# Performance work log

Hardware: AMD Instinct MI355X
Metric: run time of the kernel (lower is better)

The kernel has to match this reference:

```python
import jax, jax.numpy as jnp
import numpy as np

WIN = 16
SIGMA = 1.5
DATA_RANGE = 255.0
C1 = (0.01 * DATA_RANGE) ** 2
C2 = (0.03 * DATA_RANGE) ** 2
MSE_W = 0.7
SSIM_W = 0.3


def _gauss_window(channels):
    # 16x16 gaussian window, sigma=1.5, normalized to sum 1
    coords = np.arange(WIN, dtype=np.float32) - (WIN - 1) / 2.0
    g = np.exp(-(coords ** 2) / (2.0 * SIGMA ** 2))
    g = g / g.sum()
    w2d = np.outer(g, g)  # [16,16]
    w = np.broadcast_to(w2d, (channels, 1, WIN, WIN)).copy()
    return jnp.asarray(w)


def _depthwise_conv(x, w):
    # x: [B,C,H,W], w: [C,1,k,k] depthwise, VALID padding
    return jax.lax.conv_general_dilated(
        x, w, window_strides=(1, 1), padding='VALID',
        dimension_numbers=('NCHW', 'OIHW', 'NCHW'),
        feature_group_count=x.shape[1])


def _ssim(img1, img2):
    # images assumed in [0,255] (PIL-equivalent range)
    C = img1.shape[1]
    w = _gauss_window(C).astype(img1.dtype)
    mu1 = _depthwise_conv(img1, w)
    mu2 = _depthwise_conv(img2, w)
    mu1_sq = mu1 * mu1
    mu2_sq = mu2 * mu2
    mu12 = mu1 * mu2
    sigma1_sq = _depthwise_conv(img1 * img1, w) - mu1_sq
    sigma2_sq = _depthwise_conv(img2 * img2, w) - mu2_sq
    sigma12 = _depthwise_conv(img1 * img2, w) - mu12
    ssim_map = ((2.0 * mu12 + C1) * (2.0 * sigma12 + C2)) / (
        (mu1_sq + mu2_sq + C1) * (sigma1_sq + sigma2_sq + C2))
    # per-sample mean, then mean over batch (matches batch_ssim loop + .mean())
    return jnp.mean(ssim_map, axis=(1, 2, 3)).mean()


def setup_inputs() -> dict:
    key = jax.random.key(0)
    k1, k2 = jax.random.split(key)
    shape = (32, 3, 512, 512)
    output = jax.random.uniform(k1, shape, dtype=jnp.float32)
    target = jax.random.uniform(k2, shape, dtype=jnp.float32)
    return {'output': output, 'target': target}


def reference(output, target):
    mse_loss = jnp.mean((output - target) ** 2)
    # to_pil_image scales [0,1] float tensors to [0,255] uint8; SSIM computed
    # in 0-255 range with data_range=255
    ssim_val = _ssim(output * 255.0, target * 255.0)
    ssim_loss = 1.0 - ssim_val
    return mse_loss * MSE_W + ssim_loss * SSIM_W
```

## Files before the change

kernel.cpp:

```cpp
#include <hip/hip_runtime.h>
#include <math.h>
#include <string.h>

typedef __attribute__((ext_vector_type(8))) short bf16x8;
typedef __attribute__((ext_vector_type(4))) float f32x4;

namespace {
constexpr int TOUT = 32;
constexpr int IMG  = 512;
constexpr int HALO = 15;
constexpr int OUTW = IMG - HALO;
constexpr int NBLK = 16 * 16 * 96;

struct WinPk { unsigned w[8]; };

__device__ __forceinline__ unsigned prm(unsigned hi, unsigned lo) {
    return __builtin_amdgcn_perm(hi, lo, 0x07060302u);
}
}

template <bool TWO_STAGE>
__global__ __launch_bounds__(256)
void ssim_mse_kernel(const float* __restrict__ img1,
                     const float* __restrict__ img2,
                     WinPk wpk,
                     double2* __restrict__ partial,
                     double*  __restrict__ accum)
{
    __shared__ unsigned short S[4][48][48];
    __shared__ unsigned short HB[4][32][48];
    __shared__ unsigned short gt[64];
    __shared__ float red[2][4];

    const int tid = threadIdx.x;
    const int ox0 = blockIdx.x * TOUT;
    const int oy0 = blockIdx.y * TOUT;
    const size_t plane_off = (size_t)blockIdx.z * (IMG * IMG);
    const float* __restrict__ p1 = img1 + plane_off;
    const float* __restrict__ p2 = img2 + plane_off;

    float mse_local = 0.0f, ssim_local = 0.0f;

    if (tid < 16) gt[tid] = 0;
    else if (tid >= 32 && tid < 64) gt[tid] = 0;
    else if (tid == 16) {
        #pragma unroll
        for (int k = 0; k < 8; ++k)
            *(unsigned*)&gt[16 + 2 * k] = wpk.w[k];
    }

    if (tid < 192) {
        const int r  = tid >> 2;
        const int cs = tid & 3;
        const int c0 = 12 * cs;
        if (r == 47) {
            #pragma unroll
            for (int p = 0; p < 4; ++p)
                #pragma unroll
                for (int h = 0; h < 6; ++h)
                    *(unsigned*)&S[p][47][c0 + 2 * h] = 0u;
        } else {
            const int gy  = oy0 + r;
            const int gyc = gy < IMG ? gy : IMG - 1;
            const float* __restrict__ pa = p1 + (size_t)gyc * IMG;
            const float* __restrict__ pb = p2 + (size_t)gyc * IMG;
            float Af[12], Bf[12];
            if (ox0 + c0 + 12 <= IMG) {
                #pragma unroll
                for (int v = 0; v < 3; ++v) {
                    const float4 va = *(const float4*)(pa + ox0 + c0 + 4 * v);
                    const float4 vb = *(const float4*)(pb + ox0 + c0 + 4 * v);
                    Af[4*v+0] = va.x; Af[4*v+1] = va.y; Af[4*v+2] = va.z; Af[4*v+3] = va.w;
                    Bf[4*v+0] = vb.x; Bf[4*v+1] = vb.y; Bf[4*v+2] = vb.z; Bf[4*v+3] = vb.w;
                }
            } else {
                #pragma unroll
                for (int j = 0; j < 12; ++j) {
                    int gx = ox0 + c0 + j; gx = gx < IMG ? gx : IMG - 1;
                    Af[j] = pa[gx]; Bf[j] = pb[gx];
                }
            }
            if (r < TOUT) {
                #pragma unroll
                for (int j = 0; j < 12; ++j) {
                    if (c0 + j < TOUT) {
                        const float d = Af[j] - Bf[j];
                        mse_local = fmaf(d, d, mse_local);
                    }
                }
            }
            #pragma unroll
            for (int h = 0; h < 6; ++h) {
                const unsigned a0 = __float_as_uint(Af[2*h])   + 0x8000u;
                const unsigned a1 = __float_as_uint(Af[2*h+1]) + 0x8000u;
                const unsigned b0 = __float_as_uint(Bf[2*h])   + 0x8000u;
                const unsigned b1 = __float_as_uint(Bf[2*h+1]) + 0x8000u;
                const float ar0 = __uint_as_float(a0 & 0xFFFF0000u);
                const float ar1 = __uint_as_float(a1 & 0xFFFF0000u);
                const float br0 = __uint_as_float(b0 & 0xFFFF0000u);
                const float br1 = __uint_as_float(b1 & 0xFFFF0000u);
                const unsigned q0 = __float_as_uint(fmaf(ar0, ar0, br0 * br0)) + 0x8000u;
                const unsigned q1 = __float_as_uint(fmaf(ar1, ar1, br1 * br1)) + 0x8000u;
                const unsigned x0 = __float_as_uint(ar0 * br0) + 0x8000u;
                const unsigned x1 = __float_as_uint(ar1 * br1) + 0x8000u;
                unsigned wA = prm(a1, a0), wB = prm(b1, b0);
                unsigned wQ = prm(q1, q0), wX = prm(x1, x0);
                if (cs == 3 && h == 5) {
                    wA &= 0xFFFFu; wB &= 0xFFFFu; wQ &= 0xFFFFu; wX &= 0xFFFFu;
                }
                *(unsigned*)&S[0][r][c0 + 2*h] = wA;
                *(unsigned*)&S[1][r][c0 + 2*h] = wB;
                *(unsigned*)&S[2][r][c0 + 2*h] = wQ;
                *(unsigned*)&S[3][r][c0 + 2*h] = wX;
            }
        }
    }
    __syncthreads();

    const int m15 = tid & 15;
    const int q4  = (tid >> 4) & 3;
    const int wid = tid >> 6;

    bf16x8 wf;
    {
        const int base = q4 * 8 - m15 + 16;
        #pragma unroll
        for (int j = 0; j < 8; ++j)
            wf[j] = (short)gt[base + j];
    }

    {
        #pragma unroll
        for (int Mt = 0; Mt < 3; ++Mt) {
            #pragma unroll
            for (int Nt = 0; Nt < 2; ++Nt) {
                const bf16x8 af =
                    *(const bf16x8*)&S[wid][Mt * 16 + m15][Nt * 16 + q4 * 8];
                f32x4 c = {0.f, 0.f, 0.f, 0.f};
                c = __builtin_amdgcn_mfma_f32_16x16x32_bf16(af, wf, c, 0, 0, 0);
                const unsigned lo = prm(__float_as_uint(c[1]) + 0x8000u,
                                        __float_as_uint(c[0]) + 0x8000u);
                const unsigned hi = prm(__float_as_uint(c[3]) + 0x8000u,
                                        __float_as_uint(c[2]) + 0x8000u);
                uint2 wv; wv.x = lo; wv.y = hi;
                *(uint2*)&HB[wid][Nt * 16 + m15][Mt * 16 + q4 * 4] = wv;
            }
        }
    }
    __syncthreads();

    {
        const int Rt = wid >> 1, Ct = wid & 1;
        const int ko = Rt * 16 + q4 * 8;
        const f32x4 z = {0.f, 0.f, 0.f, 0.f};
        const bf16x8 f0 = *(const bf16x8*)&HB[0][Ct * 16 + m15][ko];
        const bf16x8 f1 = *(const bf16x8*)&HB[1][Ct * 16 + m15][ko];
        const bf16x8 f2 = *(const bf16x8*)&HB[2][Ct * 16 + m15][ko];
        const bf16x8 f3 = *(const bf16x8*)&HB[3][Ct * 16 + m15][ko];
        const f32x4 M1 = __builtin_amdgcn_mfma_f32_16x16x32_bf16(wf, f0, z, 0, 0, 0);
        const f32x4 M2 = __builtin_amdgcn_mfma_f32_16x16x32_bf16(wf, f1, z, 0, 0, 0);
        const f32x4 Qm = __builtin_amdgcn_mfma_f32_16x16x32_bf16(wf, f2, z, 0, 0, 0);
        const f32x4 Xm = __builtin_amdgcn_mfma_f32_16x16x32_bf16(wf, f3, z, 0, 0, 0);

        const float C1u = 1.0e-4f;
        const float C2u = 9.0e-4f;
        const int ocol  = ox0 + Ct * 16 + m15;
        const int orow0 = oy0 + Rt * 16 + q4 * 4;
        #pragma unroll
        for (int g = 0; g < 4; ++g) {
            const float mu1  = M1[g], mu2 = M2[g];
            const float mu12 = mu1 * mu2;
            const float musq = fmaf(mu1, mu1, mu2 * mu2);
            const float sgq  = Qm[g] - musq;
            const float sg12 = Xm[g] - mu12;
            const float num  = fmaf(2.0f, mu12, C1u) * fmaf(2.0f, sg12, C2u);
            const float den  = (musq + C1u) * (sgq + C2u);
            const float val  = num * __builtin_amdgcn_rcpf(den);
            if (ocol < OUTW && (orow0 + g) < OUTW) ssim_local += val;
        }
    }

    #pragma unroll
    for (int off = 32; off > 0; off >>= 1) {
        mse_local  += __shfl_down(mse_local,  off, 64);
        ssim_local += __shfl_down(ssim_local, off, 64);
    }
    if ((tid & 63) == 0) { red[0][wid] = mse_local; red[1][wid] = ssim_local; }
    __syncthreads();
    if (tid == 0) {
        const double m = (double)red[0][0] + (double)red[0][1]
                       + (double)red[0][2] + (double)red[0][3];
        const double s = (double)red[1][0] + (double)red[1][1]
                       + (double)red[1][2] + (double)red[1][3];
        if (TWO_STAGE) {
            const int bid = (int)blockIdx.x
                          + 16 * ((int)blockIdx.y + 16 * (int)blockIdx.z);
            partial[bid] = make_double2(m, s);
        } else {
            atomicAdd(&accum[0], m);
            atomicAdd(&accum[1], s);
        }
    }
}

__global__ __launch_bounds__(1024) void reduce_kernel(
    const double2* __restrict__ partial,
    float* __restrict__ out)
{
    __shared__ double sm[16], ss[16];
    const int tid = threadIdx.x;
    double m = 0.0, s = 0.0;
    #pragma unroll
    for (int k = 0; k < 24; ++k) {
        const double2 p = partial[tid + 1024 * k];
        m += p.x; s += p.y;
    }
    #pragma unroll
    for (int off = 32; off > 0; off >>= 1) {
        m += __shfl_down(m, off, 64);
        s += __shfl_down(s, off, 64);
    }
    if ((tid & 63) == 0) { sm[tid >> 6] = m; ss[tid >> 6] = s; }
    __syncthreads();
    if (tid == 0) {
        double M = 0.0, S = 0.0;
        #pragma unroll
        for (int w = 0; w < 16; ++w) { M += sm[w]; S += ss[w]; }
        const double mse  = M / 25165824.0;
        const double ssim = S / 23712864.0;
        out[0] = (float)(0.7 * mse + 0.3 * (1.0 - ssim));
    }
}

__global__ void finalize_kernel(const double* __restrict__ accum,
                                float* __restrict__ out)
{
    const double mse  = accum[0] / 25165824.0;
    const double ssim = accum[1] / 23712864.0;
    out[0] = (float)(0.7 * mse + 0.3 * (1.0 - ssim));
}

extern "C" void kernel_launch(void* const* d_in, const int* in_sizes, int n_in,
                              void* d_out, int out_size, void* d_ws, size_t ws_size,
                              hipStream_t stream) {
    const float* img1 = (const float*)d_in[0];
    const float* img2 = (const float*)d_in[1];
    float* out = (float*)d_out;

    WinPk wpk;
    {
        double g[16], s = 0.0;
        for (int i = 0; i < 16; ++i) {
            const double c = (double)i - 7.5;
            g[i] = exp(-(c * c) / 4.5);
            s += g[i];
        }
        unsigned short h[16];
        for (int i = 0; i < 16; ++i) {
            const float gf = (float)(g[i] / s);
            unsigned u;
            memcpy(&u, &gf, 4);
            u += 0x7FFFu + ((u >> 16) & 1u);
            h[i] = (unsigned short)(u >> 16);
        }
        for (int k = 0; k < 8; ++k)
            wpk.w[k] = (unsigned)h[2 * k] | ((unsigned)h[2 * k + 1] << 16);
    }

    dim3 grid(16, 16, 96);
    if (ws_size >= (size_t)NBLK * sizeof(double2)) {
        double2* partial = (double2*)d_ws;
        ssim_mse_kernel<true><<<grid, dim3(256), 0, stream>>>(
            img1, img2, wpk, partial, nullptr);
        reduce_kernel<<<1, dim3(1024), 0, stream>>>(partial, out);
    } else {
        double* accum = (double*)d_ws;
        hipMemsetAsync(d_ws, 0, 2 * sizeof(double), stream);
        ssim_mse_kernel<false><<<grid, dim3(256), 0, stream>>>(
            img1, img2, wpk, nullptr, accum);
        finalize_kernel<<<1, 1, 0, stream>>>(accum, out);
    }
}
```

Baseline: 245.7 us.

## Alias horizontal-pass buffer onto input tile and widen staging stores

Drops the separate HB shared buffer and writes the horizontal-pass results back into the S tile in place. The reads of the S rows each wave needs are ordered ahead of its overlapping writes, which lowers shared memory per block, and launch bounds now request 8 blocks per CU. The staging loop is rebalanced so 288 work items each load 8 columns and write 128-bit LDS stores instead of 32-bit ones, spreading the load across all 256 threads. The in-place aliasing depends on each wave touching only its own plane and on careful read/write ordering, and the occupancy hint may force register spills.

```diff
diff --git a/kernel.cpp b/kernel.cpp
--- a/kernel.cpp
+++ b/kernel.cpp
@@ -20,7 +20,7 @@
 }
 
 template <bool TWO_STAGE>
-__global__ __launch_bounds__(256)
+__global__ __launch_bounds__(256, 8)
 void ssim_mse_kernel(const float* __restrict__ img1,
                      const float* __restrict__ img2,
                      WinPk wpk,
@@ -28,7 +28,6 @@
                      double*  __restrict__ accum)
 {
     __shared__ unsigned short S[4][48][48];
-    __shared__ unsigned short HB[4][32][48];
     __shared__ unsigned short gt[64];
     __shared__ float red[2][4];
 
@@ -49,48 +48,48 @@
             *(unsigned*)&gt[16 + 2 * k] = wpk.w[k];
     }
 
-    if (tid < 192) {
-        const int r  = tid >> 2;
-        const int cs = tid & 3;
-        const int c0 = 12 * cs;
+    for (int it = tid; it < 288; it += 256) {
+        const int r   = (int)((unsigned)it / 6u);
+        const int cs8 = it - 6 * r;
+        const int c0  = 8 * cs8;
         if (r == 47) {
-            #pragma unroll
-            for (int p = 0; p < 4; ++p)
-                #pragma unroll
-                for (int h = 0; h < 6; ++h)
-                    *(unsigned*)&S[p][47][c0 + 2 * h] = 0u;
+            const uint4 z = make_uint4(0u, 0u, 0u, 0u);
+            *(uint4*)&S[0][47][c0] = z;
+            *(uint4*)&S[1][47][c0] = z;
+            *(uint4*)&S[2][47][c0] = z;
+            *(uint4*)&S[3][47][c0] = z;
         } else {
             const int gy  = oy0 + r;
             const int gyc = gy < IMG ? gy : IMG - 1;
             const float* __restrict__ pa = p1 + (size_t)gyc * IMG;
             const float* __restrict__ pb = p2 + (size_t)gyc * IMG;
-            float Af[12], Bf[12];
-            if (ox0 + c0 + 12 <= IMG) {
-                #pragma unroll
-                for (int v = 0; v < 3; ++v) {
-                    const float4 va = *(const float4*)(pa + ox0 + c0 + 4 * v);
-                    const float4 vb = *(const float4*)(pb + ox0 + c0 + 4 * v);
-                    Af[4*v+0] = va.x; Af[4*v+1] = va.y; Af[4*v+2] = va.z; Af[4*v+3] = va.w;
-                    Bf[4*v+0] = vb.x; Bf[4*v+1] = vb.y; Bf[4*v+2] = vb.z; Bf[4*v+3] = vb.w;
-                }
+            float Af[8], Bf[8];
+            if (ox0 + c0 + 8 <= IMG) {
+                const float4 va0 = *(const float4*)(pa + ox0 + c0);
+                const float4 va1 = *(const float4*)(pa + ox0 + c0 + 4);
+                const float4 vb0 = *(const float4*)(pb + ox0 + c0);
+                const float4 vb1 = *(const float4*)(pb + ox0 + c0 + 4);
+                Af[0] = va0.x; Af[1] = va0.y; Af[2] = va0.z; Af[3] = va0.w;
+                Af[4] = va1.x; Af[5] = va1.y; Af[6] = va1.z; Af[7] = va1.w;
+                Bf[0] = vb0.x; Bf[1] = vb0.y; Bf[2] = vb0.z; Bf[3] = vb0.w;
+                Bf[4] = vb1.x; Bf[5] = vb1.y; Bf[6] = vb1.z; Bf[7] = vb1.w;
             } else {
                 #pragma unroll
-                for (int j = 0; j < 12; ++j) {
+                for (int j = 0; j < 8; ++j) {
                     int gx = ox0 + c0 + j; gx = gx < IMG ? gx : IMG - 1;
                     Af[j] = pa[gx]; Bf[j] = pb[gx];
                 }
             }
-            if (r < TOUT) {
+            if (r < TOUT && cs8 < 4) {
                 #pragma unroll
-                for (int j = 0; j < 12; ++j) {
-                    if (c0 + j < TOUT) {
-                        const float d = Af[j] - Bf[j];
-                        mse_local = fmaf(d, d, mse_local);
-                    }
+                for (int j = 0; j < 8; ++j) {
+                    const float d = Af[j] - Bf[j];
+                    mse_local = fmaf(d, d, mse_local);
                 }
             }
+            unsigned wA[4], wB[4], wQ[4], wX[4];
             #pragma unroll
-            for (int h = 0; h < 6; ++h) {
+            for (int h = 0; h < 4; ++h) {
                 const unsigned a0 = __float_as_uint(Af[2*h])   + 0x8000u;
                 const unsigned a1 = __float_as_uint(Af[2*h+1]) + 0x8000u;
                 const unsigned b0 = __float_as_uint(Bf[2*h])   + 0x8000u;
@@ -103,16 +102,22 @@
                 const unsigned q1 = __float_as_uint(fmaf(ar1, ar1, br1 * br1)) + 0x8000u;
                 const unsigned x0 = __float_as_uint(ar0 * br0) + 0x8000u;
                 const unsigned x1 = __float_as_uint(ar1 * br1) + 0x8000u;
-                unsigned wA = prm(a1, a0), wB = prm(b1, b0);
-                unsigned wQ = prm(q1, q0), wX = prm(x1, x0);
-                if (cs == 3 && h == 5) {
-                    wA &= 0xFFFFu; wB &= 0xFFFFu; wQ &= 0xFFFFu; wX &= 0xFFFFu;
-                }
-                *(unsigned*)&S[0][r][c0 + 2*h] = wA;
-                *(unsigned*)&S[1][r][c0 + 2*h] = wB;
-                *(unsigned*)&S[2][r][c0 + 2*h] = wQ;
-                *(unsigned*)&S[3][r][c0 + 2*h] = wX;
-            }
+                wA[h] = prm(a1, a0); wB[h] = prm(b1, b0);
+                wQ[h] = prm(q1, q0); wX[h] = prm(x1, x0);
+            }
+            if (cs8 == 5) {
+                wA[3] &= 0xFFFFu; wB[3] &= 0xFFFFu;
+                wQ[3] &= 0xFFFFu; wX[3] &= 0xFFFFu;
+            }
+            uint4 vA, vB, vQ, vX;
+            vA.x = wA[0]; vA.y = wA[1]; vA.z = wA[2]; vA.w = wA[3];
+            vB.x = wB[0]; vB.y = wB[1]; vB.z = wB[2]; vB.w = wB[3];
+            vQ.x = wQ[0]; vQ.y = wQ[1]; vQ.z = wQ[2]; vQ.w = wQ[3];
+            vX.x = wX[0]; vX.y = wX[1]; vX.z = wX[2]; vX.w = wX[3];
+            *(uint4*)&S[0][r][c0] = vA;
+            *(uint4*)&S[1][r][c0] = vB;
+            *(uint4*)&S[2][r][c0] = vQ;
+            *(uint4*)&S[3][r][c0] = vX;
         }
     }
     __syncthreads();
@@ -130,22 +135,28 @@
     }
 
     {
-        #pragma unroll
-        for (int Mt = 0; Mt < 3; ++Mt) {
-            #pragma unroll
-            for (int Nt = 0; Nt < 2; ++Nt) {
-                const bf16x8 af =
-                    *(const bf16x8*)&S[wid][Mt * 16 + m15][Nt * 16 + q4 * 8];
-                f32x4 c = {0.f, 0.f, 0.f, 0.f};
-                c = __builtin_amdgcn_mfma_f32_16x16x32_bf16(af, wf, c, 0, 0, 0);
-                const unsigned lo = prm(__float_as_uint(c[1]) + 0x8000u,
-                                        __float_as_uint(c[0]) + 0x8000u);
-                const unsigned hi = prm(__float_as_uint(c[3]) + 0x8000u,
-                                        __float_as_uint(c[2]) + 0x8000u);
-                uint2 wv; wv.x = lo; wv.y = hi;
-                *(uint2*)&HB[wid][Nt * 16 + m15][Mt * 16 + q4 * 4] = wv;
-            }
-        }
+        auto hstep = [&](const bf16x8 af, const int Mt, const int Nt) {
+            f32x4 c = {0.f, 0.f, 0.f, 0.f};
+            c = __builtin_amdgcn_mfma_f32_16x16x32_bf16(af, wf, c, 0, 0, 0);
+            const unsigned lo = prm(__float_as_uint(c[1]) + 0x8000u,
+                                    __float_as_uint(c[0]) + 0x8000u);
+            const unsigned hi = prm(__float_as_uint(c[3]) + 0x8000u,
+                                    __float_as_uint(c[2]) + 0x8000u);
+            uint2 wv; wv.x = lo; wv.y = hi;
+            *(uint2*)&S[wid][Nt * 16 + m15][Mt * 16 + q4 * 4] = wv;
+        };
+        const bf16x8 a00 = *(const bf16x8*)&S[wid][     m15][     q4 * 8];
+        const bf16x8 a01 = *(const bf16x8*)&S[wid][     m15][16 + q4 * 8];
+        const bf16x8 a10 = *(const bf16x8*)&S[wid][16 + m15][     q4 * 8];
+        const bf16x8 a11 = *(const bf16x8*)&S[wid][16 + m15][16 + q4 * 8];
+        hstep(a00, 0, 0);
+        hstep(a01, 0, 1);
+        hstep(a10, 1, 0);
+        hstep(a11, 1, 1);
+        const bf16x8 a20 = *(const bf16x8*)&S[wid][32 + m15][     q4 * 8];
+        const bf16x8 a21 = *(const bf16x8*)&S[wid][32 + m15][16 + q4 * 8];
+        hstep(a20, 2, 0);
+        hstep(a21, 2, 1);
     }
     __syncthreads();
 
@@ -153,10 +164,10 @@
         const int Rt = wid >> 1, Ct = wid & 1;
         const int ko = Rt * 16 + q4 * 8;
         const f32x4 z = {0.f, 0.f, 0.f, 0.f};
-        const bf16x8 f0 = *(const bf16x8*)&HB[0][Ct * 16 + m15][ko];
-        const bf16x8 f1 = *(const bf16x8*)&HB[1][Ct * 16 + m15][ko];
-        const bf16x8 f2 = *(const bf16x8*)&HB[2][Ct * 16 + m15][ko];
-        const bf16x8 f3 = *(const bf16x8*)&HB[3][Ct * 16 + m15][ko];
+        const bf16x8 f0 = *(const bf16x8*)&S[0][Ct * 16 + m15][ko];
+        const bf16x8 f1 = *(const bf16x8*)&S[1][Ct * 16 + m15][ko];
+        const bf16x8 f2 = *(const bf16x8*)&S[2][Ct * 16 + m15][ko];
+        const bf16x8 f3 = *(const bf16x8*)&S[3][Ct * 16 + m15][ko];
         const f32x4 M1 = __builtin_amdgcn_mfma_f32_16x16x32_bf16(wf, f0, z, 0, 0, 0);
         const f32x4 M2 = __builtin_amdgcn_mfma_f32_16x16x32_bf16(wf, f1, z, 0, 0, 0);
         const f32x4 Qm = __builtin_amdgcn_mfma_f32_16x16x32_bf16(wf, f2, z, 0, 0, 0);
```

Result: faster. 232.3 us (-5.4%).
